# Optimization experiments

Measured on AMD Instinct MI355X. Metric: run time of the kernel, lower is better.

Reference implementation:

```python
import jax, jax.numpy as jnp
import numpy as np

B, S, HID = 2, 2048, 1024
NH = 16
HD = HID // NH  # 64
ROPE_BASE = 10000.0
NEG_INF = -1e9


def _rope_emb(seq_len):
    # emb = cat(sin, cos) over head_dim, shape [1, S, 1, HD]
    inv_freq = 1.0 / (ROPE_BASE ** (jnp.arange(0, HD, 2, dtype=jnp.float32) / HD))
    pos = jnp.arange(seq_len, dtype=jnp.float32)
    sincos = pos[:, None] * inv_freq[None, :]            # [S, HD/2]
    emb = jnp.concatenate([jnp.sin(sincos), jnp.cos(sincos)], axis=-1)  # [S, HD]
    return emb[None, :, None, :]


def _apply_rope(x, emb):
    # Faithful to the (quirky) torch code: cos = emb[..., 1::2], sin = emb[..., ::2]
    cos = emb[..., 1::2]
    sin = emb[..., ::2]
    xe = x[..., ::2]
    xo = x[..., 1::2]
    return jnp.concatenate([xe * cos - xo * sin, xe * sin + xo * cos], axis=-1)


def setup_inputs() -> dict:
    key = jax.random.key(0)
    ks = jax.random.split(key, 5)
    hidden_states = jax.random.normal(ks[0], (B, S, HID), dtype=jnp.float32)
    # causal additive mask, broadcast over batch/heads
    causal = jnp.tril(jnp.ones((S, S), dtype=bool))
    attention_mask = jnp.where(causal, 0.0, NEG_INF).astype(jnp.float32)[None, None]
    scale = 1.0 / np.sqrt(HID)
    w_q = jax.random.normal(ks[1], (HID, HID), dtype=jnp.float32) * scale
    w_k = jax.random.normal(ks[2], (HID, HID), dtype=jnp.float32) * scale
    w_v = jax.random.normal(ks[3], (HID, HID), dtype=jnp.float32) * scale
    w_o = jax.random.normal(ks[4], (HID, HID), dtype=jnp.float32) * scale
    return {"hidden_states": hidden_states, "attention_mask": attention_mask,
            "w_q": w_q, "w_k": w_k, "w_v": w_v, "w_o": w_o}


def reference(hidden_states, attention_mask, w_q, w_k, w_v, w_o):
    b, s, _ = hidden_states.shape
    # torch Linear: x @ W.T (W is [out, in])
    q = (hidden_states @ w_q.T).reshape(b, s, NH, HD)
    k = (hidden_states @ w_k.T).reshape(b, s, NH, HD)
    v = (hidden_states @ w_v.T).reshape(b, s, NH, HD)
    emb = _rope_emb(s)
    q = _apply_rope(q, emb)
    k = _apply_rope(k, emb)
    # [b, h, s, d]
    q = q.transpose(0, 2, 1, 3)
    k = k.transpose(0, 2, 1, 3)
    v = v.transpose(0, 2, 1, 3)
    scores = jnp.einsum('bhqd,bhkd->bhqk', q, k) / np.sqrt(HD)
    scores = scores + attention_mask
    attn = jax.nn.softmax(scores, axis=-1)
    out = jnp.einsum('bhqk,bhkd->bhqd', attn, v)
    out = out.transpose(0, 2, 1, 3).reshape(b, s, HID)
    return out @ w_o.T
```

## Files before the change

kernel.cpp:

```cpp
#include <hip/hip_runtime.h>
#include <hip/hip_bf16.h>
#include <math.h>

typedef unsigned short u16;
typedef unsigned int   u32;
typedef unsigned long long u64;
typedef __attribute__((ext_vector_type(8))) short bf16x8;
typedef __attribute__((ext_vector_type(4))) short bf16x4;
typedef __attribute__((ext_vector_type(4))) float f32x4;

#define B_   2
#define S_   2048
#define HID_ 1024
#define NH_  16
#define HD_  64
#define MR_  (B_*S_)

#define QSCALE 0.1803368801111137f
#define MBIAS 32.0f

__device__ __forceinline__ u16 f2bf(float f) {
  union { float f; u32 u; } x; x.f = f;
  u32 r = x.u + 0x7fffu + ((x.u >> 16) & 1u);
  return (u16)(r >> 16);
}
__device__ __forceinline__ void gload16(const void* g, void* l) {
  __builtin_amdgcn_global_load_lds(
      (const __attribute__((address_space(1))) u32*)g,
      (__attribute__((address_space(3))) u32*)l, 16, 0, 0);
}

__global__ void k_cvt_all(const float* __restrict__ hs, const float* __restrict__ wq,
                          const float* __restrict__ wk, const float* __restrict__ wv,
                          const float* __restrict__ wo, ushort4* __restrict__ dst) {
  int i = blockIdx.x * blockDim.x + threadIdx.x;
  const float4* src;
  int idx;
  if (i < 1048576) {
    src = (const float4*)hs; idx = i;
  } else {
    int j = i - 1048576;
    int w = j >> 18; idx = j & 262143;
    src = (const float4*)(w == 0 ? wq : w == 1 ? wk : w == 2 ? wv : wo);
  }
  float4 v = src[idx];
  ushort4 o;
  o.x = f2bf(v.x); o.y = f2bf(v.y); o.z = f2bf(v.z); o.w = f2bf(v.w);
  dst[i] = o;
}

__global__ void k_rope_table(float2* __restrict__ tab) {
  int t = blockIdx.x * blockDim.x + threadIdx.x;
  int p = t >> 5, j = t & 31;
  double fp = (double)p;
  double c, s;
  if (j < 16) {
    s = sin(fp * pow(10000.0, -(2.0 * j) / 32.0));
    c = sin(fp * pow(10000.0, -(2.0 * j + 1.0) / 32.0));
  } else {
    s = cos(fp * pow(10000.0, -(2.0 * j - 32.0) / 32.0));
    c = cos(fp * pow(10000.0, -(2.0 * j - 31.0) / 32.0));
  }
  tab[p * 32 + j] = make_float2((float)c, (float)s);
}

template <int MODE, int BM>
__global__ __launch_bounds__(512) void k_gemm_bt(
    const u16* __restrict__ A,
    const u16* __restrict__ W0, const u16* __restrict__ W1, const u16* __restrict__ W2,
    u16* __restrict__ O0, u16* __restrict__ O1, u16* __restrict__ O2,
    float* __restrict__ OF, const float2* __restrict__ tab, int K) {
  constexpr int WR = BM / 4;
  constexpr int MI = BM / 64;
  __shared__ __align__(16) u16 Al[2][BM * 64];
  __shared__ __align__(16) u16 Bl[2][128 * 64];

  int tid = threadIdx.x;
  int lane = tid & 63, wave = tid >> 6;
  int m0 = blockIdx.y * BM;
  int nt0 = blockIdx.x * 128;
  int wi = nt0 >> 10;
  const u16* W = (wi == 0) ? W0 : (wi == 1 ? W1 : W2);
  int n0 = nt0 & 1023;
  int wm = wave >> 1, wn = wave & 1;
  int lg = lane >> 4, lr = lane & 15;

  f32x4 acc[MI][4];
  const f32x4 vz = {0.f, 0.f, 0.f, 0.f};
#pragma unroll
  for (int i = 0; i < MI; ++i)
#pragma unroll
    for (int j = 0; j < 4; ++j) acc[i][j] = vz;

  auto STAGE = [&](int t_, int bs_) {
    int k0 = t_ * 64;
#pragma unroll
    for (int it = 0; it < BM / 64; ++it) {
      int c = it * 512 + tid;
      int row = c >> 3;
      int cw = (c & 7) ^ (row & 7);
      gload16(&A[(size_t)(m0 + row) * K + k0 + cw * 8], &Al[bs_][(it * 512 + wave * 64) * 8]);
    }
#pragma unroll
    for (int it = 0; it < 2; ++it) {
      int c = it * 512 + tid;
      int row = c >> 3;
      int cw = (c & 7) ^ (row & 7);
      gload16(&W[(size_t)(n0 + row) * K + k0 + cw * 8], &Bl[bs_][(it * 512 + wave * 64) * 8]);
    }
  };

  int nkt = K >> 6;
  STAGE(0, 0);

  for (int t = 0; t < nkt; ++t) {
    int cur = t & 1;
    if (t + 1 < nkt) {
      STAGE(t + 1, cur ^ 1);
      if (MODE == 0) asm volatile("s_waitcnt vmcnt(4)" ::: "memory");
      else           asm volatile("s_waitcnt vmcnt(3)" ::: "memory");
    } else {
      asm volatile("s_waitcnt vmcnt(0)" ::: "memory");
    }
    __builtin_amdgcn_s_barrier();
    __builtin_amdgcn_sched_barrier(0);

#pragma unroll
    for (int kk = 0; kk < 2; ++kk) {
      bf16x8 af[MI], bfr[4];
#pragma unroll
      for (int mi = 0; mi < MI; ++mi) {
        int row = wm * WR + mi * 16 + lr;
        int ci = (kk * 4 + lg) ^ (row & 7);
        af[mi] = *(const bf16x8*)&Al[cur][row * 64 + ci * 8];
      }
#pragma unroll
      for (int ni = 0; ni < 4; ++ni) {
        int row = wn * 64 + ni * 16 + lr;
        int ci = (kk * 4 + lg) ^ (row & 7);
        bfr[ni] = *(const bf16x8*)&Bl[cur][row * 64 + ci * 8];
      }
      __builtin_amdgcn_s_setprio(1);
#pragma unroll
      for (int mi = 0; mi < MI; ++mi)
#pragma unroll
        for (int ni = 0; ni < 4; ++ni)
          acc[mi][ni] = __builtin_amdgcn_mfma_f32_16x16x32_bf16(af[mi], bfr[ni], acc[mi][ni], 0, 0, 0);
      __builtin_amdgcn_s_setprio(0);
    }
    __builtin_amdgcn_sched_barrier(0);
    __builtin_amdgcn_s_barrier();
  }

  if (MODE == 1) {
#pragma unroll
    for (int mi = 0; mi < MI; ++mi)
#pragma unroll
      for (int ni = 0; ni < 4; ++ni)
#pragma unroll
        for (int r = 0; r < 4; ++r) {
          int grow = m0 + wm * WR + mi * 16 + lg * 4 + r;
          int gcol = n0 + wn * 64 + ni * 16 + lr;
          OF[(size_t)grow * 1024 + gcol] = acc[mi][ni][r];
        }
    return;
  }

  if (wi == 2) {
#pragma unroll
    for (int mi = 0; mi < MI; ++mi) {
      int grow0 = m0 + wm * WR + mi * 16 + lg * 4;
      int bb = grow0 >> 11;
      int s = grow0 & 2047;
#pragma unroll
      for (int ni = 0; ni < 4; ++ni) {
        int gcol = n0 + wn * 64 + ni * 16 + lr;
        int h = gcol >> 6, dd = gcol & 63;
        u64 pk = (u64)f2bf(acc[mi][ni][0]) |
                 ((u64)f2bf(acc[mi][ni][1]) << 16) |
                 ((u64)f2bf(acc[mi][ni][2]) << 32) |
                 ((u64)f2bf(acc[mi][ni][3]) << 48);
        *(u64*)&O2[((size_t)(bb * NH_ + h) * HD_ + dd) * S_ + s] = pk;
      }
    }
  } else {
    u16* OB = wi ? O1 : O0;
    float sc = wi ? 1.0f : QSCALE;
#pragma unroll
    for (int mi = 0; mi < MI; ++mi) {
#pragma unroll
      for (int ni = 0; ni < 4; ++ni) {
        int gcol = n0 + wn * 64 + ni * 16 + lr;
        int h = gcol >> 6;
        int j = (gcol & 63) >> 1;
        bool even = !(gcol & 1);
        int ocol = h * 64 + (even ? j : 32 + j);
#pragma unroll
        for (int r = 0; r < 4; ++r) {
          float val = acc[mi][ni][r];
          float pv = __shfl_xor(val, 1);
          int grow = m0 + wm * WR + mi * 16 + lg * 4 + r;
          int s = grow & 2047;
          float2 cs = tab[s * 32 + j];
          float xe = even ? val : pv;
          float xo = even ? pv : val;
          float res = even ? (xe * cs.x - xo * cs.y) : (xe * cs.y + xo * cs.x);
          OB[(size_t)grow * 1024 + ocol] = f2bf(res * sc);
        }
      }
    }
  }
}

__global__ __launch_bounds__(256, 4) void k_attn(
    const u16* __restrict__ Q, const u16* __restrict__ Kr, const u16* __restrict__ VT,
    u16* __restrict__ O) {
  __shared__ __align__(16) u16 Kl[2][64 * 64];
  __shared__ __align__(16) u16 Vl[2][64 * 64];

  int tid = threadIdx.x, lane = tid & 63, wave = tid >> 6;
  int id = blockIdx.x;
  int qt = 31 - (id >> 5);
  int bh = id & 31;
  int b = bh >> 4, h = bh & 15;
  int lg = lane >> 4, lr = lane & 15;
  int bS = b * S_;
  int nkt = qt + 1;
  int q0 = qt * 64 + wave * 16;

  const u16* vtb = &VT[(size_t)bh * HD_ * S_];
  int l8 = lane >> 3, l7 = lane & 7;
  int sl = l7 ^ l8;

  auto STAGE = [&](int kt_, int bs_) {
#pragma unroll
    for (int it = 0; it < 2; ++it) {
      int rb = wave * 16 + it * 8;
      int r = rb + l8;
      gload16(&Kr[(size_t)(bS + kt_ * 64 + r) * HID_ + h * HD_ + sl * 8],
              &Kl[bs_][rb * 64]);
      gload16(&vtb[(size_t)r * S_ + kt_ * 64 + sl * 8],
              &Vl[bs_][rb * 64]);
    }
  };

  STAGE(0, 0);

  bf16x8 qf[2];
#pragma unroll
  for (int kk = 0; kk < 2; ++kk)
    qf[kk] = *(const bf16x8*)
        &Q[(size_t)(bS + q0 + lr) * HID_ + h * HD_ + kk * 32 + lg * 8];

  f32x4 acc[4];
  const f32x4 vz = {0.f, 0.f, 0.f, 0.f};
#pragma unroll
  for (int df = 0; df < 4; ++df) acc[df] = vz;
  float l_ = 0.f;

  for (int kt = 0; kt < nkt; ++kt) {
    int cur = kt & 1;
    if (kt + 1 < nkt) {
      STAGE(kt + 1, cur ^ 1);
      asm volatile("s_waitcnt vmcnt(4)" ::: "memory");
    } else {
      asm volatile("s_waitcnt vmcnt(0)" ::: "memory");
    }
    __builtin_amdgcn_s_barrier();
    __builtin_amdgcn_sched_barrier(0);

    bf16x8 kfr[4][2];
#pragma unroll
    for (int kf = 0; kf < 4; ++kf) {
      int row = kf * 16 + lr;
#pragma unroll
      for (int kk = 0; kk < 2; ++kk) {
        int ci = (kk * 4 + lg) ^ (row & 7);
        kfr[kf][kk] = *(const bf16x8*)&Kl[cur][row * 64 + ci * 8];
      }
    }

    f32x4 st[4];
#pragma unroll
    for (int kf = 0; kf < 4; ++kf) st[kf] = vz;
    __builtin_amdgcn_s_setprio(1);
#pragma unroll
    for (int kk = 0; kk < 2; ++kk)
#pragma unroll
      for (int kf = 0; kf < 4; ++kf)
        st[kf] = __builtin_amdgcn_mfma_f32_16x16x32_bf16(
            kfr[kf][kk], qf[kk], st[kf], 0, 0, 0);
    __builtin_amdgcn_s_setprio(0);

    if (kt == qt) {
      int qg = q0 + lr;
#pragma unroll
      for (int kf = 0; kf < 4; ++kf)
#pragma unroll
        for (int r = 0; r < 4; ++r) {
          int kg = kt * 64 + kf * 16 + lg * 4 + r;
          if (kg > qg) st[kf][r] = -1e30f;
        }
    }

    float ts = 0.f;
    bf16x4 pb[4];
#pragma unroll
    for (int kf = 0; kf < 4; ++kf) {
#pragma unroll
      for (int r = 0; r < 4; ++r) {
        float e = __builtin_amdgcn_exp2f(st[kf][r] - MBIAS);
        st[kf][r] = e;
        ts += e;
      }
      u32 w0, w1;
      asm("v_cvt_pk_bf16_f32 %0, %1, %2" : "=v"(w0) : "v"(st[kf][0]), "v"(st[kf][1]));
      asm("v_cvt_pk_bf16_f32 %0, %1, %2" : "=v"(w1) : "v"(st[kf][2]), "v"(st[kf][3]));
      union { u32 u[2]; bf16x4 v; } pk;
      pk.u[0] = w0; pk.u[1] = w1;
      pb[kf] = pk.v;
    }
    l_ += ts;

    __builtin_amdgcn_s_setprio(1);
#pragma unroll
    for (int df = 0; df < 4; ++df) {
      int row = df * 16 + lr;
#pragma unroll
      for (int kf = 0; kf < 4; ++kf) {
        int slot = (kf * 2 + (lg >> 1)) ^ (row & 7);
        bf16x4 vfr = *(const bf16x4*)&Vl[cur][row * 64 + slot * 8 + (lg & 1) * 4];
        acc[df] = __builtin_amdgcn_mfma_f32_16x16x16bf16_1k(
            vfr, pb[kf], acc[df], 0, 0, 0);
      }
    }
    __builtin_amdgcn_s_setprio(0);

    __builtin_amdgcn_sched_barrier(0);
    __builtin_amdgcn_s_barrier();
  }

  l_ += __shfl_xor(l_, 16);
  l_ += __shfl_xor(l_, 32);
  float inv = 1.0f / l_;
  int grow = bS + q0 + lr;
#pragma unroll
  for (int df = 0; df < 4; ++df) {
    u64 pk = (u64)f2bf(acc[df][0] * inv) |
             ((u64)f2bf(acc[df][1] * inv) << 16) |
             ((u64)f2bf(acc[df][2] * inv) << 32) |
             ((u64)f2bf(acc[df][3] * inv) << 48);
    *(u64*)&O[(size_t)grow * HID_ + h * HD_ + df * 16 + lg * 4] = pk;
  }
}

extern "C" void kernel_launch(void* const* d_in, const int* in_sizes, int n_in,
                              void* d_out, int out_size, void* d_ws, size_t ws_size,
                              hipStream_t stream) {
  const float* hs = (const float*)d_in[0];
  const float* wq = (const float*)d_in[2];
  const float* wk = (const float*)d_in[3];
  const float* wv = (const float*)d_in[4];
  const float* wo = (const float*)d_in[5];
  float* out = (float*)d_out;

  char* ws = (char*)d_ws;
  const size_t P = (size_t)MR_ * HID_ * 2;
  u16* Xb  = (u16*)(ws);
  u16* Wqb = (u16*)(ws + P);
  u16* Wkb = (u16*)(ws + P + (size_t)HID_ * HID_ * 2);
  u16* Wvb = (u16*)(ws + P + (size_t)HID_ * HID_ * 4);
  u16* Wob = (u16*)(ws + P + (size_t)HID_ * HID_ * 6);
  u16* q_r = (u16*)(ws + 2 * P);
  u16* k_r = (u16*)(ws + 3 * P);
  u16* vt  = (u16*)(ws + 4 * P);
  float2* tab = (float2*)(ws + 5 * P);
  u16* attn_o = Xb;

  k_cvt_all<<<8192, 256, 0, stream>>>(hs, wq, wk, wv, wo, (ushort4*)ws);
  k_rope_table<<<256, 256, 0, stream>>>(tab);

  k_gemm_bt<0, 128><<<dim3(24, 32), 512, 0, stream>>>(
      Xb, Wqb, Wkb, Wvb, q_r, k_r, vt, nullptr, tab, HID_);

  k_attn<<<1024, 256, 0, stream>>>(q_r, k_r, vt, attn_o);

  k_gemm_bt<1, 64><<<dim3(8, 64), 512, 0, stream>>>(
      attn_o, Wob, Wob, Wob, nullptr, nullptr, nullptr, out, nullptr, HID_);
}
```

Before: 115.2 us.

## Fuse rope table into convert kernel, XCD-aware tile mapping, single-barrier pipeline

Merges the rope table kernel into the conversion kernel so there is one launch fewer. The GEMM grids become 1D, with a block-to-tile mapping chosen so that blocks sharing an XCD reuse the same weight column tiles in L2. The GEMM and attention loops now issue the next stage's prefetch after a single wait-all plus barrier, dropping the trailing barrier. The cost is that each step waits on all outstanding loads instead of a partial vmcnt, which may expose more load latency.

```diff
diff --git a/kernel.cpp b/kernel.cpp
--- a/kernel.cpp
+++ b/kernel.cpp
@@ -32,8 +32,25 @@
 
 __global__ void k_cvt_all(const float* __restrict__ hs, const float* __restrict__ wq,
                           const float* __restrict__ wk, const float* __restrict__ wv,
-                          const float* __restrict__ wo, ushort4* __restrict__ dst) {
-  int i = blockIdx.x * blockDim.x + threadIdx.x;
+                          const float* __restrict__ wo, ushort4* __restrict__ dst,
+                          float2* __restrict__ tab) {
+  int bid = blockIdx.x;
+  if (bid >= 8192) {
+    int t = (bid - 8192) * blockDim.x + threadIdx.x;
+    int p = t >> 5, j = t & 31;
+    double fp = (double)p;
+    double c, s;
+    if (j < 16) {
+      s = sin(fp * pow(10000.0, -(2.0 * j) / 32.0));
+      c = sin(fp * pow(10000.0, -(2.0 * j + 1.0) / 32.0));
+    } else {
+      s = cos(fp * pow(10000.0, -(2.0 * j - 32.0) / 32.0));
+      c = cos(fp * pow(10000.0, -(2.0 * j - 31.0) / 32.0));
+    }
+    tab[p * 32 + j] = make_float2((float)c, (float)s);
+    return;
+  }
+  int i = bid * blockDim.x + threadIdx.x;
   const float4* src;
   int idx;
   if (i < 1048576) {
@@ -47,21 +64,6 @@
   ushort4 o;
   o.x = f2bf(v.x); o.y = f2bf(v.y); o.z = f2bf(v.z); o.w = f2bf(v.w);
   dst[i] = o;
-}
-
-__global__ void k_rope_table(float2* __restrict__ tab) {
-  int t = blockIdx.x * blockDim.x + threadIdx.x;
-  int p = t >> 5, j = t & 31;
-  double fp = (double)p;
-  double c, s;
-  if (j < 16) {
-    s = sin(fp * pow(10000.0, -(2.0 * j) / 32.0));
-    c = sin(fp * pow(10000.0, -(2.0 * j + 1.0) / 32.0));
-  } else {
-    s = cos(fp * pow(10000.0, -(2.0 * j - 32.0) / 32.0));
-    c = cos(fp * pow(10000.0, -(2.0 * j - 31.0) / 32.0));
-  }
-  tab[p * 32 + j] = make_float2((float)c, (float)s);
 }
 
 template <int MODE, int BM>
@@ -77,8 +79,17 @@
 
   int tid = threadIdx.x;
   int lane = tid & 63, wave = tid >> 6;
-  int m0 = blockIdx.y * BM;
-  int nt0 = blockIdx.x * 128;
+  int id = blockIdx.x;
+  int m0, nt0;
+  if (MODE == 0) {
+    int xcd = id & 7, g = id >> 3;
+    int j = g >> 5, mt = g & 31;
+    nt0 = (xcd + 8 * j) * 128;
+    m0 = mt * 128;
+  } else {
+    nt0 = (id & 7) * 128;
+    m0 = (id >> 3) * 64;
+  }
   int wi = nt0 >> 10;
   const u16* W = (wi == 0) ? W0 : (wi == 1 ? W1 : W2);
   int n0 = nt0 & 1023;
@@ -115,15 +126,10 @@
 
   for (int t = 0; t < nkt; ++t) {
     int cur = t & 1;
-    if (t + 1 < nkt) {
-      STAGE(t + 1, cur ^ 1);
-      if (MODE == 0) asm volatile("s_waitcnt vmcnt(4)" ::: "memory");
-      else           asm volatile("s_waitcnt vmcnt(3)" ::: "memory");
-    } else {
-      asm volatile("s_waitcnt vmcnt(0)" ::: "memory");
-    }
+    asm volatile("s_waitcnt vmcnt(0)" ::: "memory");
     __builtin_amdgcn_s_barrier();
     __builtin_amdgcn_sched_barrier(0);
+    if (t + 1 < nkt) STAGE(t + 1, cur ^ 1);
 
 #pragma unroll
     for (int kk = 0; kk < 2; ++kk) {
@@ -148,8 +154,6 @@
           acc[mi][ni] = __builtin_amdgcn_mfma_f32_16x16x32_bf16(af[mi], bfr[ni], acc[mi][ni], 0, 0, 0);
       __builtin_amdgcn_s_setprio(0);
     }
-    __builtin_amdgcn_sched_barrier(0);
-    __builtin_amdgcn_s_barrier();
   }
 
   if (MODE == 1) {
@@ -260,14 +264,10 @@
 
   for (int kt = 0; kt < nkt; ++kt) {
     int cur = kt & 1;
-    if (kt + 1 < nkt) {
-      STAGE(kt + 1, cur ^ 1);
-      asm volatile("s_waitcnt vmcnt(4)" ::: "memory");
-    } else {
-      asm volatile("s_waitcnt vmcnt(0)" ::: "memory");
-    }
+    asm volatile("s_waitcnt vmcnt(0)" ::: "memory");
     __builtin_amdgcn_s_barrier();
     __builtin_amdgcn_sched_barrier(0);
+    if (kt + 1 < nkt) STAGE(kt + 1, cur ^ 1);
 
     bf16x8 kfr[4][2];
 #pragma unroll
@@ -335,9 +335,6 @@
       }
     }
     __builtin_amdgcn_s_setprio(0);
-
-    __builtin_amdgcn_sched_barrier(0);
-    __builtin_amdgcn_s_barrier();
   }
 
   l_ += __shfl_xor(l_, 16);
@@ -377,14 +374,13 @@
   float2* tab = (float2*)(ws + 5 * P);
   u16* attn_o = Xb;
 
-  k_cvt_all<<<8192, 256, 0, stream>>>(hs, wq, wk, wv, wo, (ushort4*)ws);
-  k_rope_table<<<256, 256, 0, stream>>>(tab);
-
-  k_gemm_bt<0, 128><<<dim3(24, 32), 512, 0, stream>>>(
+  k_cvt_all<<<8448, 256, 0, stream>>>(hs, wq, wk, wv, wo, (ushort4*)ws, tab);
+
+  k_gemm_bt<0, 128><<<768, 512, 0, stream>>>(
       Xb, Wqb, Wkb, Wvb, q_r, k_r, vt, nullptr, tab, HID_);
 
   k_attn<<<1024, 256, 0, stream>>>(q_r, k_r, vt, attn_o);
 
-  k_gemm_bt<1, 64><<<dim3(8, 64), 512, 0, stream>>>(
+  k_gemm_bt<1, 64><<<512, 512, 0, stream>>>(
       attn_o, Wob, Wob, Wob, nullptr, nullptr, nullptr, out, nullptr, HID_);
 }
```

Measured after the change: 120.8 us. 4.9% more time.
